# Kernel tuning notes

Measured on AMD Instinct MI355X. Metric: run time of the kernel, lower is better.

Reference implementation:

```python
import jax, jax.numpy as jnp
import numpy as np

W_BIT = 4
OUT_F = 11008
IN_F = 4096
K = 16
TOKENS = 2048


def unpack_sign(qweight, out_f, in_f):
    """qweight: [w_bit, out_f*in_f//8] ints in [0,256). Each byte packs 8 signs,
    LSB-first: bit j of byte m -> element m*8+j; bit 1 -> +1, bit 0 -> -1.
    Returns float32 signs of shape [w_bit, out_f, in_f]."""
    shifts = jnp.arange(8, dtype=qweight.dtype)
    bits = (qweight[..., None] >> shifts) & 1  # [w_bit, n_bytes, 8]
    sign = (2 * bits - 1).astype(jnp.float32)
    return sign.reshape(qweight.shape[0], out_f, in_f)


def setup_inputs() -> dict:
    key = jax.random.key(0)
    k1, k2, k3, k4 = jax.random.split(key, 4)
    x = jax.random.normal(k1, (TOKENS, IN_F), dtype=jnp.float32)
    qweight = jax.random.randint(k2, (W_BIT, OUT_F * IN_F // 8), 0, 256, dtype=jnp.int32)
    u = jax.random.normal(k3, (W_BIT, OUT_F, K), dtype=jnp.float32) * 0.05
    vt = jax.random.normal(k4, (W_BIT, K, IN_F), dtype=jnp.float32) * 0.05
    return {"x": x, "qweight": qweight, "u": u, "vt": vt}


def reference(x, qweight, u, vt):
    # Reconstruct w = sum_i sign_i * (u_i @ vt_i), then y = x @ w.T  (forward_l0)
    sign = unpack_sign(qweight, OUT_F, IN_F)                  # [b, O, I]
    low_rank = jnp.einsum('bok,bki->boi', u, vt)              # [b, O, I]
    w = jnp.sum(sign * low_rank, axis=0)                      # [O, I]
    return x @ w.T                                            # [T, O]
```

## Files before the change

### kernel.cpp

```cpp
#include <hip/hip_runtime.h>
#include <cstdint>
#include <cstddef>

#define TOKENS 2048
#define IN_F   4096
#define OUT_F  11008
#define W_BIT  4
#define RANK   16
#define QWB    (OUT_F * IN_F / 8)

typedef unsigned short ushort_t;
typedef __attribute__((ext_vector_type(8))) short   short8;
typedef __attribute__((ext_vector_type(4))) float   floatx4;

__device__ __forceinline__ ushort_t f2bf(float f) {
  union { float f; uint32_t u; } c; c.f = f;
  uint32_t r = c.u + 0x7FFFu + ((c.u >> 16) & 1u);
  return (ushort_t)(r >> 16);
}

__device__ __forceinline__ void gl_lds16(const void* g, void* l) {
  __builtin_amdgcn_global_load_lds(
      (const __attribute__((address_space(1))) uint32_t*)g,
      (__attribute__((address_space(3))) uint32_t*)l, 16, 0, 0);
}

__global__ __launch_bounds__(256) void k_cvt_x(const float* __restrict__ x,
                                               ushort_t* __restrict__ xb) {
  int idx = blockIdx.x * 256 + threadIdx.x;
  float4 v = ((const float4*)x)[idx];
  ushort4 r;
  r.x = f2bf(v.x); r.y = f2bf(v.y); r.z = f2bf(v.z); r.w = f2bf(v.w);
  ((ushort4*)xb)[idx] = r;
}

#define N_U  (W_BIT * OUT_F * RANK)
#define N_VT (W_BIT * RANK * IN_F)
__global__ __launch_bounds__(256) void k_prep_uv(const float* __restrict__ u,
                                                 const float* __restrict__ vt,
                                                 ushort_t* __restrict__ ub,
                                                 ushort_t* __restrict__ vtT) {
  int idx = blockIdx.x * 256 + threadIdx.x;
  if (idx < N_U) {
    ub[idx] = f2bf(u[idx]);
  } else {
    int e = idx - N_U;
    int b = e >> 16;
    int r = e & 65535;
    int k = r >> 12;
    int i = r & 4095;
    vtT[((size_t)b * IN_F + i) * RANK + k] = f2bf(vt[e]);
  }
}

__global__ __launch_bounds__(256) void k_build_w(const int* __restrict__ qw,
                                                 const ushort_t* __restrict__ ub,
                                                 const ushort_t* __restrict__ vtT,
                                                 ushort_t* __restrict__ w) {
  __shared__ int qs[W_BIT * 128 * 20];
  const int tid = threadIdx.x;
  const int ob = blockIdx.x / (IN_F / 128);
  const int ib = blockIdx.x % (IN_F / 128);
  const int o0 = ob * 128, i0 = ib * 128;
  const int lane = tid & 63, wv = tid >> 6;
  const int wm = (wv >> 1) * 64, wn = (wv & 1) * 64;
  const int l16 = lane & 15, q = lane >> 4;
  const bool qlo = (q < 2);
  const int koff = (q & 1) * 8;
  const short8 zf = (short8)0;

  #pragma unroll
  for (int n = 0; n < 8; ++n) {
    int c = n * 256 + tid;
    int b = c >> 9, rem = c & 511;
    int row = rem >> 2, part = rem & 3;
    int4 v = *(const int4*)(qw + (size_t)b * QWB +
                            (size_t)(o0 + row) * (IN_F / 8) + (i0 >> 3) + part * 4);
    *(int4*)&qs[(b * 128 + row) * 20 + part * 4] = v;
  }

  floatx4 acc[16];
  #pragma unroll
  for (int i = 0; i < 16; ++i) acc[i] = (floatx4){0.f, 0.f, 0.f, 0.f};

  const int qc_base = (wn >> 3) + (l16 >> 3);
  const int bit = l16 & 7;

  __syncthreads();

  #pragma unroll
  for (int b = 0; b < W_BIT; ++b) {
    short8 af[4], bfr[4];
    #pragma unroll
    for (int mi = 0; mi < 4; ++mi) {
      short8 v = *(const short8*)&ub[((size_t)b * OUT_F + o0 + wm + mi * 16 + l16) * RANK + koff];
      af[mi] = qlo ? v : zf;
    }
    #pragma unroll
    for (int ni = 0; ni < 4; ++ni) {
      short8 v = *(const short8*)&vtT[((size_t)b * IN_F + i0 + wn + ni * 16 + l16) * RANK + koff];
      bfr[ni] = qlo ? v : zf;
    }

    #pragma unroll
    for (int mi = 0; mi < 4; ++mi) {
      floatx4 p[4];
      #pragma unroll
      for (int ni = 0; ni < 4; ++ni)
        p[ni] = __builtin_amdgcn_mfma_f32_16x16x32_bf16(
            af[mi], bfr[ni], (floatx4){0.f, 0.f, 0.f, 0.f}, 0, 0, 0);
      #pragma unroll
      for (int v4 = 0; v4 < 4; ++v4) {
        const int o_loc = wm + mi * 16 + q * 4 + v4;
        const int* qrow = &qs[(b * 128 + o_loc) * 20];
        #pragma unroll
        for (int ni = 0; ni < 4; ++ni) {
          int qv = qrow[qc_base + ni * 2];
          float pv = p[ni][v4];
          acc[mi * 4 + ni][v4] += ((qv >> bit) & 1) ? pv : -pv;
        }
      }
    }
  }

  #pragma unroll
  for (int mi = 0; mi < 4; ++mi) {
    #pragma unroll
    for (int v4 = 0; v4 < 4; ++v4) {
      const int o = o0 + wm + mi * 16 + q * 4 + v4;
      #pragma unroll
      for (int ni = 0; ni < 4; ++ni)
        w[(size_t)o * IN_F + i0 + wn + ni * 16 + l16] = f2bf(acc[mi * 4 + ni][v4]);
    }
  }
}

__global__ __launch_bounds__(256) void k_gemm_bt(const ushort_t* __restrict__ A,
                                                 const ushort_t* __restrict__ B,
                                                 float* __restrict__ C) {
  __shared__ ushort_t As[128 * 32];
  __shared__ ushort_t Bs[128 * 32];
  const int tid = threadIdx.x;
  const int bm = blockIdx.x & 15;
  const int bn = blockIdx.x >> 4;
  const int lane = tid & 63, wv = tid >> 6;
  const int wm = (wv >> 1) * 64, wn = (wv & 1) * 64;
  const int l16 = lane & 15, q = lane >> 4;

  floatx4 acc[16];
  #pragma unroll
  for (int i = 0; i < 16; ++i) acc[i] = (floatx4){0.f, 0.f, 0.f, 0.f};

  const int c0 = tid,        row0 = c0 >> 2, col0 = (c0 & 3) << 3;
  const int c1 = 256 + tid,  row1 = c1 >> 2, col1 = (c1 & 3) << 3;
  const int ldsb0 = (tid & 192) * 16;
  const int ldsb1 = (256 + (tid & 192)) * 16;
  const size_t ar = (size_t)(bm * 128), br = (size_t)(bn * 128);

  for (int kt = 0; kt < IN_F; kt += 32) {
    gl_lds16(A + (ar + row0) * IN_F + kt + col0, (char*)As + ldsb0);
    gl_lds16(A + (ar + row1) * IN_F + kt + col1, (char*)As + ldsb1);
    gl_lds16(B + (br + row0) * IN_F + kt + col0, (char*)Bs + ldsb0);
    gl_lds16(B + (br + row1) * IN_F + kt + col1, (char*)Bs + ldsb1);
    __syncthreads();

    short8 af[4], bf[4];
    #pragma unroll
    for (int mi = 0; mi < 4; ++mi)
      af[mi] = *(const short8*)&As[(wm + mi * 16 + l16) * 32 + q * 8];
    #pragma unroll
    for (int ni = 0; ni < 4; ++ni)
      bf[ni] = *(const short8*)&Bs[(wn + ni * 16 + l16) * 32 + q * 8];
    #pragma unroll
    for (int mi = 0; mi < 4; ++mi)
      #pragma unroll
      for (int ni = 0; ni < 4; ++ni)
        acc[mi * 4 + ni] =
            __builtin_amdgcn_mfma_f32_16x16x32_bf16(af[mi], bf[ni], acc[mi * 4 + ni], 0, 0, 0);
    __syncthreads();
  }

  #pragma unroll
  for (int mi = 0; mi < 4; ++mi) {
    #pragma unroll
    for (int ni = 0; ni < 4; ++ni) {
      #pragma unroll
      for (int v = 0; v < 4; ++v) {
        int r = bm * 128 + wm + mi * 16 + q * 4 + v;
        int c = bn * 128 + wn + ni * 16 + l16;
        C[(size_t)r * OUT_F + c] = acc[mi * 4 + ni][v];
      }
    }
  }
}

extern "C" void kernel_launch(void* const* d_in, const int* in_sizes, int n_in,
                              void* d_out, int out_size, void* d_ws, size_t ws_size,
                              hipStream_t stream) {
  (void)in_sizes; (void)n_in; (void)out_size; (void)ws_size;
  const float* x  = (const float*)d_in[0];
  const int*   qw = (const int*)d_in[1];
  const float* u  = (const float*)d_in[2];
  const float* vt = (const float*)d_in[3];
  float* out = (float*)d_out;

  char* wsp = (char*)d_ws;
  ushort_t* xb  = (ushort_t*)wsp;
  ushort_t* wb  = (ushort_t*)(wsp + (size_t)TOKENS * IN_F * 2);
  ushort_t* ubf = (ushort_t*)(wsp + (size_t)TOKENS * IN_F * 2 + (size_t)OUT_F * IN_F * 2);
  ushort_t* vtT = (ushort_t*)(wsp + (size_t)TOKENS * IN_F * 2 + (size_t)OUT_F * IN_F * 2 +
                              (size_t)N_U * 2);

  k_cvt_x<<<TOKENS * IN_F / 1024, 256, 0, stream>>>(x, xb);
  k_prep_uv<<<(N_U + N_VT) / 256, 256, 0, stream>>>(u, vt, ubf, vtT);
  k_build_w<<<(OUT_F / 128) * (IN_F / 128), 256, 0, stream>>>(qw, ubf, vtT, wb);
  k_gemm_bt<<<16 * (OUT_F / 128), 256, 0, stream>>>(xb, wb, out);
}
```

Measured before the change: 524.3 us.

## Pipeline GEMM with 4-stage LDS ring, 128x256 tiles, swizzle and XCD remap

Rewrites the main bf16 GEMM to use 512-thread blocks with 128x256 output tiles and a 4-slot LDS ring buffer filled by direct global-to-LDS loads three stages ahead. Fragments for the next step are double-buffered in registers, waits use explicit vmcnt counts, and MFMA issue runs at raised priority. It adds an XOR swizzle to avoid LDS bank conflicts and remaps block IDs across the 8 XCDs for cache locality. This hides global load latency and cuts the per-iteration syncthreads stalls of the old single-buffered loop, at the cost of larger LDS use (96KB) that limits occupancy.

```diff
diff --git a/kernel.cpp b/kernel.cpp
--- a/kernel.cpp
+++ b/kernel.cpp
@@ -135,50 +135,86 @@
   }
 }
 
-__global__ __launch_bounds__(256) void k_gemm_bt(const ushort_t* __restrict__ A,
+#define NT (IN_F / 32)
+__global__ __launch_bounds__(512) void k_gemm_bt(const ushort_t* __restrict__ A,
                                                  const ushort_t* __restrict__ B,
                                                  float* __restrict__ C) {
-  __shared__ ushort_t As[128 * 32];
-  __shared__ ushort_t Bs[128 * 32];
+  __shared__ __attribute__((aligned(16))) char lds[98304];
   const int tid = threadIdx.x;
-  const int bm = blockIdx.x & 15;
-  const int bn = blockIdx.x >> 4;
+  const int wg = (blockIdx.x & 7) * 86 + (blockIdx.x >> 3);
+  const int bm = wg & 15;
+  const int bn = wg >> 4;
   const int lane = tid & 63, wv = tid >> 6;
-  const int wm = (wv >> 1) * 64, wn = (wv & 1) * 64;
+  const int wm = wv >> 2, wn = wv & 3;
   const int l16 = lane & 15, q = lane >> 4;
-
-  floatx4 acc[16];
-  #pragma unroll
-  for (int i = 0; i < 16; ++i) acc[i] = (floatx4){0.f, 0.f, 0.f, 0.f};
-
-  const int c0 = tid,        row0 = c0 >> 2, col0 = (c0 & 3) << 3;
-  const int c1 = 256 + tid,  row1 = c1 >> 2, col1 = (c1 & 3) << 3;
-  const int ldsb0 = (tid & 192) * 16;
-  const int ldsb1 = (256 + (tid & 192)) * 16;
-  const size_t ar = (size_t)(bm * 128), br = (size_t)(bn * 128);
-
-  for (int kt = 0; kt < IN_F; kt += 32) {
-    gl_lds16(A + (ar + row0) * IN_F + kt + col0, (char*)As + ldsb0);
-    gl_lds16(A + (ar + row1) * IN_F + kt + col1, (char*)As + ldsb1);
-    gl_lds16(B + (br + row0) * IN_F + kt + col0, (char*)Bs + ldsb0);
-    gl_lds16(B + (br + row1) * IN_F + kt + col1, (char*)Bs + ldsb1);
-    __syncthreads();
-
-    short8 af[4], bf[4];
-    #pragma unroll
-    for (int mi = 0; mi < 4; ++mi)
-      af[mi] = *(const short8*)&As[(wm + mi * 16 + l16) * 32 + q * 8];
-    #pragma unroll
-    for (int ni = 0; ni < 4; ++ni)
-      bf[ni] = *(const short8*)&Bs[(wn + ni * 16 + l16) * 32 + q * 8];
-    #pragma unroll
-    for (int mi = 0; mi < 4; ++mi)
-      #pragma unroll
-      for (int ni = 0; ni < 4; ++ni)
-        acc[mi * 4 + ni] =
-            __builtin_amdgcn_mfma_f32_16x16x32_bf16(af[mi], bf[ni], acc[mi * 4 + ni], 0, 0, 0);
-    __syncthreads();
-  }
+  const int sQ = q ^ ((l16 >> 1) & 3);
+
+  const size_t ar = (size_t)bm * 128, br = (size_t)bn * 256;
+  const int qsrc = (tid & 3) ^ ((tid >> 3) & 3);
+  const ushort_t* Ae  = A + (ar + (tid >> 2)) * IN_F + qsrc * 8;
+  const ushort_t* B0e = B + (br + (tid >> 2)) * IN_F + qsrc * 8;
+  const ushort_t* B1e = B + (br + 128 + (tid >> 2)) * IN_F + qsrc * 8;
+  char* ldsw = lds + (tid & 448) * 16;
+  const int aFrag = (wm * 64 + l16) * 64 + sQ * 16;
+  const int bFrag = (wn * 64 + l16) * 64 + sQ * 16;
+
+  floatx4 acc[4][4];
+  #pragma unroll
+  for (int mi = 0; mi < 4; ++mi)
+    #pragma unroll
+    for (int ni = 0; ni < 4; ++ni) acc[mi][ni] = (floatx4){0.f, 0.f, 0.f, 0.f};
+
+  short8 a0[4], b0[4], a1[4], b1[4];
+
+#define STAGE(tt) do {                                                       \
+    const int _sl = (tt) & 3; const size_t _k0 = (size_t)(tt) * 32;          \
+    gl_lds16(Ae + _k0,  ldsw + _sl * 8192);                                  \
+    gl_lds16(B0e + _k0, ldsw + 32768 + _sl * 16384);                         \
+    gl_lds16(B1e + _k0, ldsw + 32768 + _sl * 16384 + 8192);                  \
+  } while (0)
+
+#define LDFRAGS(AF, BF, sl) do {                                             \
+    const char* _ab = lds + (sl) * 8192;                                     \
+    const char* _bb = lds + 32768 + (sl) * 16384;                            \
+    _Pragma("unroll") for (int mi = 0; mi < 4; ++mi)                         \
+      AF[mi] = *(const short8*)(_ab + aFrag + mi * 1024);                    \
+    _Pragma("unroll") for (int ni = 0; ni < 4; ++ni)                         \
+      BF[ni] = *(const short8*)(_bb + bFrag + ni * 1024);                    \
+  } while (0)
+
+#define BODY(u, AI, BI, AM, BMr) do {                                        \
+    asm volatile("" ::: "memory");                                           \
+    __builtin_amdgcn_s_barrier();         \
+    asm volatile("" ::: "memory");                                           \
+    if ((u) + 3 < NT) STAGE((u) + 3);              \
+    if ((u) + 3 < NT)      asm volatile("s_waitcnt vmcnt(6)" ::: "memory");  \
+    else if ((u) + 2 < NT) asm volatile("s_waitcnt vmcnt(3)" ::: "memory");  \
+    else                   asm volatile("s_waitcnt vmcnt(0)" ::: "memory");  \
+    __builtin_amdgcn_s_barrier();            \
+    asm volatile("" ::: "memory");                                           \
+    LDFRAGS(AI, BI, ((u) + 1) & 3);          \
+    __builtin_amdgcn_s_setprio(1);                                           \
+    _Pragma("unroll") for (int mi = 0; mi < 4; ++mi)                         \
+      _Pragma("unroll") for (int ni = 0; ni < 4; ++ni)                       \
+        acc[mi][ni] = __builtin_amdgcn_mfma_f32_16x16x32_bf16(               \
+            AM[mi], BMr[ni], acc[mi][ni], 0, 0, 0);                          \
+    __builtin_amdgcn_s_setprio(0);                                           \
+  } while (0)
+
+  STAGE(0); STAGE(1); STAGE(2);
+  asm volatile("s_waitcnt vmcnt(6)" ::: "memory");
+  __builtin_amdgcn_s_barrier();
+  asm volatile("" ::: "memory");
+  LDFRAGS(a0, b0, 0);
+
+  for (int t = 0; t < NT; t += 2) {
+    BODY(t,     a1, b1, a0, b0);
+    BODY(t + 1, a0, b0, a1, b1);
+  }
+
+#undef STAGE
+#undef LDFRAGS
+#undef BODY
 
   #pragma unroll
   for (int mi = 0; mi < 4; ++mi) {
@@ -186,9 +222,9 @@
     for (int ni = 0; ni < 4; ++ni) {
       #pragma unroll
       for (int v = 0; v < 4; ++v) {
-        int r = bm * 128 + wm + mi * 16 + q * 4 + v;
-        int c = bn * 128 + wn + ni * 16 + l16;
-        C[(size_t)r * OUT_F + c] = acc[mi * 4 + ni][v];
+        int r = bm * 128 + wm * 64 + mi * 16 + q * 4 + v;
+        int c = bn * 256 + wn * 64 + ni * 16 + l16;
+        C[(size_t)r * OUT_F + c] = acc[mi][ni][v];
       }
     }
   }
@@ -214,5 +250,5 @@
   k_cvt_x<<<TOKENS * IN_F / 1024, 256, 0, stream>>>(x, xb);
   k_prep_uv<<<(N_U + N_VT) / 256, 256, 0, stream>>>(u, vt, ubf, vtT);
   k_build_w<<<(OUT_F / 128) * (IN_F / 128), 256, 0, stream>>>(qw, ubf, vtT, wb);
-  k_gemm_bt<<<16 * (OUT_F / 128), 256, 0, stream>>>(xb, wb, out);
-}
+  k_gemm_bt<<<16 * (OUT_F / 256), 512, 0, stream>>>(xb, wb, out);
+}
```

Measured after the change: 458.2 us. 1.14x faster.
